# Kernel tuning notes

Measured on AMD Instinct MI355X. Metric: run time of the kernel, lower is better.

The kernel has to match this reference:

```python
import jax, jax.numpy as jnp
import numpy as np
import math

EPS_LN = 1e-5
SCALE = 16.0  # cosine_sim_scale


def layer_norm(x, g):
    mean = jnp.mean(x, axis=-1, keepdims=True)
    var = jnp.var(x, axis=-1, keepdims=True)  # biased, matches unbiased=False
    return (x - mean) * jax.lax.rsqrt(var + EPS_LN) * g


def l2norm(t):
    n = jnp.linalg.norm(t, axis=-1, keepdims=True)
    return t / jnp.maximum(n, 1e-12)


def setup_inputs() -> dict:
    key = jax.random.key(0)
    ks = jax.random.split(key, 4)
    b, n, dim, h, dh = 4, 2048, 1024, 8, 64
    inner = h * dh
    x = jax.random.normal(ks[0], (b, n, dim), dtype=jnp.float32)
    Wq = jax.random.normal(ks[1], (dim, inner), dtype=jnp.float32) * (dim ** -0.5)
    Wkv = jax.random.normal(ks[2], (dim, 2 * dh), dtype=jnp.float32) * (dim ** -0.5)
    Wout = jax.random.normal(ks[3], (inner, dim), dtype=jnp.float32) * (inner ** -0.5)
    norm_g = jnp.ones((dim,), dtype=jnp.float32)
    out_norm_g = jnp.ones((dim,), dtype=jnp.float32)
    return {"x": x, "norm_g": norm_g, "Wq": Wq, "Wkv": Wkv, "Wout": Wout,
            "out_norm_g": out_norm_g}


def reference(x, norm_g, Wq, Wkv, Wout, out_norm_g):
    b, n, dim = x.shape
    h = 8
    dh = Wkv.shape[-1] // 2
    xn = layer_norm(x, norm_g)
    q = xn @ Wq                      # [b, n, h*dh]
    kv = xn @ Wkv                    # [b, n, 2*dh]
    k, v = kv[..., :dh], kv[..., dh:]
    q = q.reshape(b, n, h, dh).transpose(0, 2, 1, 3)  # [b, h, n, dh]
    q = q * SCALE                    # cancelled by l2norm, kept for fidelity
    q = l2norm(q)
    k = l2norm(k)
    rs = math.sqrt(SCALE)
    q = q * rs
    k = k * rs
    sim = jnp.einsum('bhid,bjd->bhij', q, k)          # [b, h, n, n]
    attn = jax.nn.softmax(sim.astype(jnp.float32), axis=-1).astype(sim.dtype)
    out = jnp.einsum('bhij,bjd->bhid', attn, v)       # [b, h, n, dh]
    out = out.transpose(0, 2, 1, 3).reshape(b, n, h * dh)
    out = out @ Wout
    return layer_norm(out, out_norm_g)
```

## Files before the change

### kernel.cpp

```cpp
#include <hip/hip_runtime.h>
#include <hip/hip_bf16.h>

typedef __attribute__((ext_vector_type(8))) short short8;
typedef __attribute__((ext_vector_type(4))) float floatx4;

__device__ __forceinline__ float bf2f(ushort u) {
    return __uint_as_float(((unsigned int)u) << 16);
}
__device__ __forceinline__ ushort f2bf(float f) {
    unsigned int u = __float_as_uint(f);
    unsigned int r = (u + 0x7FFFu + ((u >> 16) & 1u)) >> 16;
    return (ushort)r;
}
__device__ __forceinline__ unsigned int pk2(float a, float b) {
    union { __hip_bfloat162 h; unsigned int u; } cv;
    cv.h = __float22bfloat162_rn(make_float2(a, b));
    return cv.u;
}
__device__ __forceinline__ float scrub(float v, float lim) {
    return fminf(fmaxf(v, -lim), lim);
}

__device__ __forceinline__ bool detect_bf16(const ushort* __restrict__ probe) {
    const int lane = threadIdx.x & 63;
    ushort u = probe[(lane & 31) * 2];
    int e = (u >> 7) & 0xFF;
    bool pl = (e >= 117) && (e <= 131) && (lane < 32);
    return __popcll(__ballot(pl)) >= 16;
}

__global__ __launch_bounds__(256) void ln1_kernel(const void* __restrict__ xin,
                                                  const void* __restrict__ gin,
                                                  ushort* __restrict__ out,
                                                  const ushort* __restrict__ probe) {
    const bool ib = detect_bf16(probe);
    const int row = blockIdx.x;
    const int tid = threadIdx.x;

    float v0, v1, v2, v3, g0, g1, g2, g3;
    if (ib) {
        uint2 u = *(const uint2*)((const ushort*)xin + (size_t)row * 1024 + tid * 4);
        v0 = bf2f((ushort)(u.x & 0xFFFF)); v1 = bf2f((ushort)(u.x >> 16));
        v2 = bf2f((ushort)(u.y & 0xFFFF)); v3 = bf2f((ushort)(u.y >> 16));
        uint2 gu = *(const uint2*)((const ushort*)gin + tid * 4);
        g0 = bf2f((ushort)(gu.x & 0xFFFF)); g1 = bf2f((ushort)(gu.x >> 16));
        g2 = bf2f((ushort)(gu.y & 0xFFFF)); g3 = bf2f((ushort)(gu.y >> 16));
    } else {
        float4 xv = *(const float4*)((const float*)xin + (size_t)row * 1024 + tid * 4);
        v0 = xv.x; v1 = xv.y; v2 = xv.z; v3 = xv.w;
        float4 gv = *(const float4*)((const float*)gin + tid * 4);
        g0 = gv.x; g1 = gv.y; g2 = gv.z; g3 = gv.w;
    }
    v0 = scrub(v0, 1e8f); v1 = scrub(v1, 1e8f); v2 = scrub(v2, 1e8f); v3 = scrub(v3, 1e8f);
    g0 = scrub(g0, 1e8f); g1 = scrub(g1, 1e8f); g2 = scrub(g2, 1e8f); g3 = scrub(g3, 1e8f);

    float s  = v0 + v1 + v2 + v3;
    float sq = v0 * v0 + v1 * v1 + v2 * v2 + v3 * v3;
    #pragma unroll
    for (int off = 1; off < 64; off <<= 1) {
        s  += __shfl_xor(s, off);
        sq += __shfl_xor(sq, off);
    }
    __shared__ float red[8];
    const int w = tid >> 6, lane = tid & 63;
    if (lane == 0) { red[w] = s; red[w + 4] = sq; }
    __syncthreads();
    float S  = red[0] + red[1] + red[2] + red[3];
    float SQ = red[4] + red[5] + red[6] + red[7];

    float mean = S * (1.0f / 1024.0f);
    float var  = SQ * (1.0f / 1024.0f) - mean * mean;
    float rstd = rsqrtf(fmaxf(var, 0.0f) + 1e-5f);

    uint2 ov;
    ov.x = pk2((v0 - mean) * rstd * g0, (v1 - mean) * rstd * g1);
    ov.y = pk2((v2 - mean) * rstd * g2, (v3 - mean) * rstd * g3);
    *(uint2*)(out + (size_t)row * 1024 + tid * 4) = ov;
}

__global__ __launch_bounds__(256) void ln2_kernel(const ushort* __restrict__ y,
                                                  const void* __restrict__ gin,
                                                  void* __restrict__ out,
                                                  const ushort* __restrict__ probe) {
    const bool ob = detect_bf16(probe);
    const int row = blockIdx.x;
    const int tid = threadIdx.x;

    uint2 u = *(const uint2*)(y + (size_t)row * 1024 + tid * 4);
    float v0 = scrub(bf2f((ushort)(u.x & 0xFFFF)), 1e8f);
    float v1 = scrub(bf2f((ushort)(u.x >> 16)),    1e8f);
    float v2 = scrub(bf2f((ushort)(u.y & 0xFFFF)), 1e8f);
    float v3 = scrub(bf2f((ushort)(u.y >> 16)),    1e8f);

    float g0, g1, g2, g3;
    if (ob) {
        uint2 gu = *(const uint2*)((const ushort*)gin + tid * 4);
        g0 = bf2f((ushort)(gu.x & 0xFFFF)); g1 = bf2f((ushort)(gu.x >> 16));
        g2 = bf2f((ushort)(gu.y & 0xFFFF)); g3 = bf2f((ushort)(gu.y >> 16));
    } else {
        float4 gv = *(const float4*)((const float*)gin + tid * 4);
        g0 = gv.x; g1 = gv.y; g2 = gv.z; g3 = gv.w;
    }
    g0 = scrub(g0, 1e8f); g1 = scrub(g1, 1e8f); g2 = scrub(g2, 1e8f); g3 = scrub(g3, 1e8f);

    float s  = v0 + v1 + v2 + v3;
    float sq = v0 * v0 + v1 * v1 + v2 * v2 + v3 * v3;
    #pragma unroll
    for (int off = 1; off < 64; off <<= 1) {
        s  += __shfl_xor(s, off);
        sq += __shfl_xor(sq, off);
    }
    __shared__ float red[8];
    const int w = tid >> 6, lane = tid & 63;
    if (lane == 0) { red[w] = s; red[w + 4] = sq; }
    __syncthreads();
    float S  = red[0] + red[1] + red[2] + red[3];
    float SQ = red[4] + red[5] + red[6] + red[7];

    float mean = S * (1.0f / 1024.0f);
    float var  = SQ * (1.0f / 1024.0f) - mean * mean;
    float rstd = rsqrtf(fmaxf(var, 0.0f) + 1e-5f);

    float o0 = (v0 - mean) * rstd * g0;
    float o1 = (v1 - mean) * rstd * g1;
    float o2 = (v2 - mean) * rstd * g2;
    float o3 = (v3 - mean) * rstd * g3;
    if (ob) {
        uint2 ov;
        ov.x = pk2(o0, o1);
        ov.y = pk2(o2, o3);
        *(uint2*)((ushort*)out + (size_t)row * 1024 + tid * 4) = ov;
    } else {
        *(float4*)((float*)out + (size_t)row * 1024 + tid * 4) = make_float4(o0, o1, o2, o3);
    }
}

__global__ __launch_bounds__(256) void transpose_kernel(const void* __restrict__ in,
                                                        ushort* __restrict__ out,
                                                        int in_rs, long long in_bs,
                                                        int out_rs, long long out_bs,
                                                        int force_bf16,
                                                        const ushort* __restrict__ probe) {
    const bool ib = force_bf16 ? true : detect_bf16(probe);
    __shared__ ushort tile[32][33];
    const int tx = threadIdx.x & 31, ty = threadIdx.x >> 5;

    #pragma unroll
    for (int rr = 0; rr < 32; rr += 8) {
        size_t idx = (size_t)blockIdx.z * in_bs + (size_t)(blockIdx.y * 32 + ty + rr) * in_rs
                   + blockIdx.x * 32 + tx;
        float v = ib ? bf2f(((const ushort*)in)[idx]) : ((const float*)in)[idx];
        tile[ty + rr][tx] = f2bf(scrub(v, 1e8f));
    }
    __syncthreads();
    ushort* op = out + (size_t)blockIdx.z * out_bs;
    #pragma unroll
    for (int rr = 0; rr < 32; rr += 8) {
        int r = blockIdx.x * 32 + ty + rr;
        int c = blockIdx.y * 32 + tx;
        op[(size_t)r * out_rs + c] = tile[tx][ty + rr];
    }
}

__global__ __launch_bounds__(256) void gemm_qkv(const ushort* __restrict__ A,
                                                const ushort* __restrict__ Bt,
                                                ushort* __restrict__ qb,
                                                ushort* __restrict__ kb,
                                                ushort* __restrict__ vt) {
    __shared__ ushort a_t[64][40];
    __shared__ ushort b_t[64][40];

    const int bx = blockIdx.x;
    const int n0 = bx * 64, m0 = blockIdx.y * 64;
    const int tid = threadIdx.x;
    const int w = tid >> 6, lane = tid & 63;
    const int fm = lane & 15, quad = lane >> 4;
    const int lrow = tid >> 2, lk = (tid & 3) * 8;
    const int K = 1024;

    const ushort* ag = A + (size_t)(m0 + lrow) * K + lk;
    const ushort* bg = Bt + (size_t)(n0 + lrow) * K + lk;

    floatx4 acc[4];
    floatx4 zero4 = {0.0f, 0.0f, 0.0f, 0.0f};
    #pragma unroll
    for (int nt = 0; nt < 4; nt++) acc[nt] = zero4;

    for (int k0 = 0; k0 < K; k0 += 32) {
        uint4 av = *(const uint4*)(ag + k0);
        uint4 bv = *(const uint4*)(bg + k0);
        __syncthreads();
        *(uint2*)&a_t[lrow][lk]     = make_uint2(av.x, av.y);
        *(uint2*)&a_t[lrow][lk + 4] = make_uint2(av.z, av.w);
        *(uint2*)&b_t[lrow][lk]     = make_uint2(bv.x, bv.y);
        *(uint2*)&b_t[lrow][lk + 4] = make_uint2(bv.z, bv.w);
        __syncthreads();

        union { uint2 u2[2]; short8 s8; } af;
        af.u2[0] = *(const uint2*)&a_t[w * 16 + fm][quad * 8];
        af.u2[1] = *(const uint2*)&a_t[w * 16 + fm][quad * 8 + 4];
        #pragma unroll
        for (int nt = 0; nt < 4; nt++) {
            union { uint2 u2[2]; short8 s8; } bf;
            bf.u2[0] = *(const uint2*)&b_t[nt * 16 + fm][quad * 8];
            bf.u2[1] = *(const uint2*)&b_t[nt * 16 + fm][quad * 8 + 4];
            acc[nt] = __builtin_amdgcn_mfma_f32_16x16x32_bf16(af.s8, bf.s8, acc[nt], 0, 0, 0);
        }
    }

    if (bx < 9) {
        float sc[4];
        #pragma unroll
        for (int r = 0; r < 4; r++) {
            float ss = acc[0][r] * acc[0][r] + acc[1][r] * acc[1][r]
                     + acc[2][r] * acc[2][r] + acc[3][r] * acc[3][r];
            ss += __shfl_xor(ss, 1);
            ss += __shfl_xor(ss, 2);
            ss += __shfl_xor(ss, 4);
            ss += __shfl_xor(ss, 8);
            sc[r] = 4.0f / fmaxf(sqrtf(ss), 1e-12f);
        }
        ushort* op;
        int rs;
        if (bx < 8) { op = qb + n0; rs = 512; }
        else        { op = kb;      rs = 64;  }
        #pragma unroll
        for (int nt = 0; nt < 4; nt++)
            #pragma unroll
            for (int r = 0; r < 4; r++)
                op[(size_t)(m0 + w * 16 + quad * 4 + r) * rs + nt * 16 + fm] =
                    f2bf(acc[nt][r] * sc[r]);
    } else {
        const int b = m0 >> 11;
        const int jb = (m0 & 2047) + w * 16 + quad * 4;
        ushort* vb = vt + (size_t)b * 64 * 2048 + jb;
        #pragma unroll
        for (int nt = 0; nt < 4; nt++) {
            uint2 pv;
            pv.x = pk2(acc[nt][0], acc[nt][1]);
            pv.y = pk2(acc[nt][2], acc[nt][3]);
            *(uint2*)(vb + (size_t)(nt * 16 + fm) * 2048) = pv;
        }
    }
}

__global__ __launch_bounds__(256) void gemm_bt(const ushort* __restrict__ A,
                                               const ushort* __restrict__ Bt,
                                               ushort* __restrict__ C,
                                               int M, int N, int K) {
    __shared__ ushort a_t[64][40];
    __shared__ ushort b_t[64][40];

    const int n0 = blockIdx.x * 64, m0 = blockIdx.y * 64;
    const int tid = threadIdx.x;
    const int w = tid >> 6, lane = tid & 63;
    const int fm = lane & 15, quad = lane >> 4;
    const int lrow = tid >> 2, lk = (tid & 3) * 8;

    const ushort* ag = A + (size_t)(m0 + lrow) * K + lk;
    const ushort* bg = Bt + (size_t)(n0 + lrow) * K + lk;

    floatx4 acc[4];
    floatx4 zero4 = {0.0f, 0.0f, 0.0f, 0.0f};
    #pragma unroll
    for (int nt = 0; nt < 4; nt++) acc[nt] = zero4;

    for (int k0 = 0; k0 < K; k0 += 32) {
        uint4 av = *(const uint4*)(ag + k0);
        uint4 bv = *(const uint4*)(bg + k0);
        __syncthreads();
        *(uint2*)&a_t[lrow][lk]     = make_uint2(av.x, av.y);
        *(uint2*)&a_t[lrow][lk + 4] = make_uint2(av.z, av.w);
        *(uint2*)&b_t[lrow][lk]     = make_uint2(bv.x, bv.y);
        *(uint2*)&b_t[lrow][lk + 4] = make_uint2(bv.z, bv.w);
        __syncthreads();

        union { uint2 u2[2]; short8 s8; } af;
        af.u2[0] = *(const uint2*)&a_t[w * 16 + fm][quad * 8];
        af.u2[1] = *(const uint2*)&a_t[w * 16 + fm][quad * 8 + 4];
        #pragma unroll
        for (int nt = 0; nt < 4; nt++) {
            union { uint2 u2[2]; short8 s8; } bf;
            bf.u2[0] = *(const uint2*)&b_t[nt * 16 + fm][quad * 8];
            bf.u2[1] = *(const uint2*)&b_t[nt * 16 + fm][quad * 8 + 4];
            acc[nt] = __builtin_amdgcn_mfma_f32_16x16x32_bf16(af.s8, bf.s8, acc[nt], 0, 0, 0);
        }
    }

    #pragma unroll
    for (int nt = 0; nt < 4; nt++)
        #pragma unroll
        for (int r = 0; r < 4; r++)
            C[(size_t)(m0 + w * 16 + quad * 4 + r) * N + n0 + nt * 16 + fm] = f2bf(acc[nt][r]);
}

__global__ __launch_bounds__(512, 4) void attn_kernel(const ushort* __restrict__ q,
                                                      const ushort* __restrict__ kb,
                                                      const ushort* __restrict__ vt,
                                                      ushort* __restrict__ out) {
    __shared__ ushort k_t[64][72];
    __shared__ ushort v_t[64][72];
    __shared__ ushort p_tile[8][16][72];

    const int i0 = blockIdx.x * 128;
    const int h = blockIdx.y, b = blockIdx.z;
    const int tid = threadIdx.x, w = tid >> 6, lane = tid & 63;
    const int fm = lane & 15, quad = lane >> 4;

    union U8 { uint4 u4; short8 s8; };

    const ushort* qbase = q + ((size_t)(b * 2048 + i0 + w * 16 + fm) * 512) + h * 64 + quad * 8;
    U8 qf0, qf1;
    qf0.u4 = *(const uint4*)qbase;
    qf1.u4 = *(const uint4*)(qbase + 32);

    floatx4 zero4 = {0.0f, 0.0f, 0.0f, 0.0f};
    floatx4 acc_o[4];
    #pragma unroll
    for (int od = 0; od < 4; od++) acc_o[od] = zero4;
    float lsum = 0.0f;

    const ushort* kbb = kb + (size_t)b * 2048 * 64;
    const ushort* vtb = vt + (size_t)b * 64 * 2048;

    const int srow = tid >> 3;
    const int sk = (tid & 7) * 8;

    for (int j0 = 0; j0 < 2048; j0 += 64) {
        uint4 ka = *(const uint4*)(kbb + (size_t)(j0 + srow) * 64 + sk);
        uint4 va = *(const uint4*)(vtb + (size_t)srow * 2048 + j0 + sk);
        __syncthreads();
        *(uint4*)&k_t[srow][sk] = ka;
        *(uint4*)&v_t[srow][sk] = va;
        __syncthreads();

        #pragma unroll
        for (int nt = 0; nt < 4; nt++) {
            U8 kb0, kb1;
            kb0.u4 = *(const uint4*)&k_t[nt * 16 + fm][quad * 8];
            kb1.u4 = *(const uint4*)&k_t[nt * 16 + fm][quad * 8 + 32];
            floatx4 st = zero4;
            st = __builtin_amdgcn_mfma_f32_16x16x32_bf16(kb0.s8, qf0.s8, st, 0, 0, 0);
            st = __builtin_amdgcn_mfma_f32_16x16x32_bf16(kb1.s8, qf1.s8, st, 0, 0, 0);
            float p0 = __expf(fminf(st[0], 16.0f) - 16.0f);
            float p1 = __expf(fminf(st[1], 16.0f) - 16.0f);
            float p2 = __expf(fminf(st[2], 16.0f) - 16.0f);
            float p3 = __expf(fminf(st[3], 16.0f) - 16.0f);
            lsum += (p0 + p1) + (p2 + p3);
            uint2 pkv;
            pkv.x = pk2(p0, p1);
            pkv.y = pk2(p2, p3);
            *(uint2*)&p_tile[w][fm][nt * 16 + quad * 4] = pkv;
        }

        U8 pb0, pb1;
        pb0.u4 = *(const uint4*)&p_tile[w][fm][quad * 8];
        pb1.u4 = *(const uint4*)&p_tile[w][fm][32 + quad * 8];

        #pragma unroll
        for (int od = 0; od < 4; od++) {
            U8 vb0, vb1;
            vb0.u4 = *(const uint4*)&v_t[od * 16 + fm][quad * 8];
            vb1.u4 = *(const uint4*)&v_t[od * 16 + fm][quad * 8 + 32];
            acc_o[od] = __builtin_amdgcn_mfma_f32_16x16x32_bf16(vb0.s8, pb0.s8, acc_o[od], 0, 0, 0);
            acc_o[od] = __builtin_amdgcn_mfma_f32_16x16x32_bf16(vb1.s8, pb1.s8, acc_o[od], 0, 0, 0);
        }
    }

    lsum += __shfl_xor(lsum, 16);
    lsum += __shfl_xor(lsum, 32);
    float li = 1.0f / fmaxf(lsum, 1e-30f);

    ushort* ob = out + (size_t)(b * 2048 + i0 + w * 16 + fm) * 512 + h * 64;
    #pragma unroll
    for (int od = 0; od < 4; od++) {
        uint2 ov;
        ov.x = pk2(acc_o[od][0] * li, acc_o[od][1] * li);
        ov.y = pk2(acc_o[od][2] * li, acc_o[od][3] * li);
        *(uint2*)(ob + od * 16 + quad * 4) = ov;
    }
}

extern "C" void kernel_launch(void* const* d_in, const int* in_sizes, int n_in,
                              void* d_out, int out_size, void* d_ws, size_t ws_size,
                              hipStream_t stream) {
    const void* x          = d_in[0];
    const void* norm_g     = d_in[1];
    const void* Wq         = d_in[2];
    const void* Wkv        = d_in[3];
    const void* Wout       = d_in[4];
    const void* out_norm_g = d_in[5];
    const ushort* probe = (const ushort*)d_in[0];
    ushort* ws = (ushort*)d_ws;

    const size_t M1 = 1024 * 1024 / 2;
    ushort* xn    = (ushort*)d_out;
    ushort* ao    = (ushort*)d_out;
    ushort* woT   = (ushort*)((char*)d_out + (8u << 20));
    ushort* qb    = ws;
    ushort* kb    = ws + 8 * M1;
    ushort* vt    = ws + 9 * M1;
    ushort* wcatT = ws + 11 * M1;
    ushort* y     = ws;

    transpose_kernel<<<dim3(16, 32, 1), 256, 0, stream>>>(Wq, wcatT, 512, 0, 1024, 0, 0, probe);
    transpose_kernel<<<dim3(4, 32, 1), 256, 0, stream>>>(Wkv, wcatT + (size_t)512 * 1024, 128, 0, 1024, 0, 0, probe);

    ln1_kernel<<<8192, 256, 0, stream>>>(x, norm_g, xn, probe);

    gemm_qkv<<<dim3(10, 128), 256, 0, stream>>>(xn, wcatT, qb, kb, vt);

    transpose_kernel<<<dim3(32, 16, 1), 256, 0, stream>>>(Wout, woT, 1024, 0, 512, 0, 0, probe);

    attn_kernel<<<dim3(16, 8, 4), 512, 0, stream>>>(qb, kb, vt, ao);

    gemm_bt<<<dim3(16, 128), 256, 0, stream>>>(ao, woT, y, 8192, 1024, 512);

    ln2_kernel<<<8192, 256, 0, stream>>>(y, out_norm_g, d_out, probe);
}
```

Before: 230.0 us.

## Fuse weight transposes into LN and attention kernels, enlarge output GEMM tiles

Weight transposes for Wq/Wkv are folded into the first layernorm launch and the Wout transpose into extra blocks of the attention launch, cutting the launch count. The output projection GEMM moves to 128x128 tiles fed by direct global-to-LDS loads. The attention loop now processes 128 keys per stage, and the clamp before exp is dropped, which relies on scores staying at or below 16 after l2norm. These changes reduce launch overhead and synchronisation per unit of work but raise LDS use per block and remove the overflow guard.

```diff
diff --git a/kernel.cpp b/kernel.cpp
--- a/kernel.cpp
+++ b/kernel.cpp
@@ -19,6 +19,10 @@
 }
 __device__ __forceinline__ float scrub(float v, float lim) {
     return fminf(fmaxf(v, -lim), lim);
+}
+__device__ __forceinline__ void glds16(const ushort* g, ushort* l) {
+    __builtin_amdgcn_global_load_lds((const __attribute__((address_space(1))) void*)g,
+                                     (__attribute__((address_space(3))) void*)l, 16, 0, 0);
 }
 
 __device__ __forceinline__ bool detect_bf16(const ushort* __restrict__ probe) {
@@ -29,14 +33,50 @@
     return __popcll(__ballot(pl)) >= 16;
 }
 
-__global__ __launch_bounds__(256) void ln1_kernel(const void* __restrict__ xin,
-                                                  const void* __restrict__ gin,
-                                                  ushort* __restrict__ out,
-                                                  const ushort* __restrict__ probe) {
+__device__ __forceinline__ void do_transpose(const void* __restrict__ in,
+                                             ushort* __restrict__ out,
+                                             int bx, int by, int in_rs, int out_rs,
+                                             bool ib, ushort* tile , int nthr) {
+    const int tx = threadIdx.x & 31, ty = threadIdx.x >> 5;
+    const int step = nthr >> 5;
+    for (int rr = 0; rr < 32; rr += step) {
+        size_t idx = (size_t)(by * 32 + ty + rr) * in_rs + bx * 32 + tx;
+        float v = ib ? bf2f(((const ushort*)in)[idx]) : ((const float*)in)[idx];
+        tile[(ty + rr) * 33 + tx] = f2bf(scrub(v, 1e8f));
+    }
+    __syncthreads();
+    for (int rr = 0; rr < 32; rr += step) {
+        int r = bx * 32 + ty + rr;
+        int c = by * 32 + tx;
+        out[(size_t)r * out_rs + c] = tile[tx * 33 + (ty + rr)];
+    }
+}
+
+__global__ __launch_bounds__(256) void prep_kernel(const void* __restrict__ xin,
+                                                   const void* __restrict__ gin,
+                                                   const void* __restrict__ Wq,
+                                                   const void* __restrict__ Wkv,
+                                                   ushort* __restrict__ xn,
+                                                   ushort* __restrict__ wcatT,
+                                                   const ushort* __restrict__ probe) {
     const bool ib = detect_bf16(probe);
-    const int row = blockIdx.x;
+    const int id = blockIdx.x;
+    __shared__ ushort tile[32 * 33];
+    __shared__ float red[8];
+
+    if (id >= 8192) {
+        if (id < 8704) {
+            int t = id - 8192;
+            do_transpose(Wq, wcatT, t & 15, t >> 4, 512, 1024, ib, tile, 256);
+        } else {
+            int t = id - 8704;
+            do_transpose(Wkv, wcatT + (size_t)512 * 1024, t & 3, t >> 2, 128, 1024, ib, tile, 256);
+        }
+        return;
+    }
+
+    const int row = id;
     const int tid = threadIdx.x;
-
     float v0, v1, v2, v3, g0, g1, g2, g3;
     if (ib) {
         uint2 u = *(const uint2*)((const ushort*)xin + (size_t)row * 1024 + tid * 4);
@@ -61,7 +101,6 @@
         s  += __shfl_xor(s, off);
         sq += __shfl_xor(sq, off);
     }
-    __shared__ float red[8];
     const int w = tid >> 6, lane = tid & 63;
     if (lane == 0) { red[w] = s; red[w + 4] = sq; }
     __syncthreads();
@@ -75,7 +114,7 @@
     uint2 ov;
     ov.x = pk2((v0 - mean) * rstd * g0, (v1 - mean) * rstd * g1);
     ov.y = pk2((v2 - mean) * rstd * g2, (v3 - mean) * rstd * g3);
-    *(uint2*)(out + (size_t)row * 1024 + tid * 4) = ov;
+    *(uint2*)(xn + (size_t)row * 1024 + tid * 4) = ov;
 }
 
 __global__ __launch_bounds__(256) void ln2_kernel(const ushort* __restrict__ y,
@@ -135,33 +174,6 @@
     }
 }
 
-__global__ __launch_bounds__(256) void transpose_kernel(const void* __restrict__ in,
-                                                        ushort* __restrict__ out,
-                                                        int in_rs, long long in_bs,
-                                                        int out_rs, long long out_bs,
-                                                        int force_bf16,
-                                                        const ushort* __restrict__ probe) {
-    const bool ib = force_bf16 ? true : detect_bf16(probe);
-    __shared__ ushort tile[32][33];
-    const int tx = threadIdx.x & 31, ty = threadIdx.x >> 5;
-
-    #pragma unroll
-    for (int rr = 0; rr < 32; rr += 8) {
-        size_t idx = (size_t)blockIdx.z * in_bs + (size_t)(blockIdx.y * 32 + ty + rr) * in_rs
-                   + blockIdx.x * 32 + tx;
-        float v = ib ? bf2f(((const ushort*)in)[idx]) : ((const float*)in)[idx];
-        tile[ty + rr][tx] = f2bf(scrub(v, 1e8f));
-    }
-    __syncthreads();
-    ushort* op = out + (size_t)blockIdx.z * out_bs;
-    #pragma unroll
-    for (int rr = 0; rr < 32; rr += 8) {
-        int r = blockIdx.x * 32 + ty + rr;
-        int c = blockIdx.y * 32 + tx;
-        op[(size_t)r * out_rs + c] = tile[tx][ty + rr];
-    }
-}
-
 __global__ __launch_bounds__(256) void gemm_qkv(const ushort* __restrict__ A,
                                                 const ushort* __restrict__ Bt,
                                                 ushort* __restrict__ qb,
@@ -244,63 +256,85 @@
     }
 }
 
-__global__ __launch_bounds__(256) void gemm_bt(const ushort* __restrict__ A,
-                                               const ushort* __restrict__ Bt,
-                                               ushort* __restrict__ C,
-                                               int M, int N, int K) {
-    __shared__ ushort a_t[64][40];
-    __shared__ ushort b_t[64][40];
-
-    const int n0 = blockIdx.x * 64, m0 = blockIdx.y * 64;
+__global__ __launch_bounds__(256) void gemm_bt128(const ushort* __restrict__ A,
+                                                  const ushort* __restrict__ Bt,
+                                                  ushort* __restrict__ C,
+                                                  int M, int N, int K) {
+    __shared__ ushort a_t[128][32];
+    __shared__ ushort b_t[128][32];
+
+    const int n0 = blockIdx.x * 128, m0 = blockIdx.y * 128;
     const int tid = threadIdx.x;
     const int w = tid >> 6, lane = tid & 63;
     const int fm = lane & 15, quad = lane >> 4;
-    const int lrow = tid >> 2, lk = (tid & 3) * 8;
-
-    const ushort* ag = A + (size_t)(m0 + lrow) * K + lk;
-    const ushort* bg = Bt + (size_t)(n0 + lrow) * K + lk;
-
-    floatx4 acc[4];
+
+    const int c0 = tid, c1 = tid + 256;
+    const ushort* ag0 = A + (size_t)(m0 + (c0 >> 2)) * K + (c0 & 3) * 8;
+    const ushort* ag1 = A + (size_t)(m0 + (c1 >> 2)) * K + (c1 & 3) * 8;
+    const ushort* bg0 = Bt + (size_t)(n0 + (c0 >> 2)) * K + (c0 & 3) * 8;
+    const ushort* bg1 = Bt + (size_t)(n0 + (c1 >> 2)) * K + (c1 & 3) * 8;
+    ushort* la0 = &a_t[0][0] + c0 * 8;
+    ushort* la1 = &a_t[0][0] + c1 * 8;
+    ushort* lb0 = &b_t[0][0] + c0 * 8;
+    ushort* lb1 = &b_t[0][0] + c1 * 8;
+
+    floatx4 acc[2][8];
     floatx4 zero4 = {0.0f, 0.0f, 0.0f, 0.0f};
     #pragma unroll
-    for (int nt = 0; nt < 4; nt++) acc[nt] = zero4;
+    for (int mt = 0; mt < 2; mt++)
+        #pragma unroll
+        for (int nt = 0; nt < 8; nt++) acc[mt][nt] = zero4;
+
+    union U8 { uint4 u4; short8 s8; };
 
     for (int k0 = 0; k0 < K; k0 += 32) {
-        uint4 av = *(const uint4*)(ag + k0);
-        uint4 bv = *(const uint4*)(bg + k0);
-        __syncthreads();
-        *(uint2*)&a_t[lrow][lk]     = make_uint2(av.x, av.y);
-        *(uint2*)&a_t[lrow][lk + 4] = make_uint2(av.z, av.w);
-        *(uint2*)&b_t[lrow][lk]     = make_uint2(bv.x, bv.y);
-        *(uint2*)&b_t[lrow][lk + 4] = make_uint2(bv.z, bv.w);
-        __syncthreads();
-
-        union { uint2 u2[2]; short8 s8; } af;
-        af.u2[0] = *(const uint2*)&a_t[w * 16 + fm][quad * 8];
-        af.u2[1] = *(const uint2*)&a_t[w * 16 + fm][quad * 8 + 4];
-        #pragma unroll
-        for (int nt = 0; nt < 4; nt++) {
-            union { uint2 u2[2]; short8 s8; } bf;
-            bf.u2[0] = *(const uint2*)&b_t[nt * 16 + fm][quad * 8];
-            bf.u2[1] = *(const uint2*)&b_t[nt * 16 + fm][quad * 8 + 4];
-            acc[nt] = __builtin_amdgcn_mfma_f32_16x16x32_bf16(af.s8, bf.s8, acc[nt], 0, 0, 0);
-        }
-    }
-
-    #pragma unroll
-    for (int nt = 0; nt < 4; nt++)
-        #pragma unroll
-        for (int r = 0; r < 4; r++)
-            C[(size_t)(m0 + w * 16 + quad * 4 + r) * N + n0 + nt * 16 + fm] = f2bf(acc[nt][r]);
+        __syncthreads();
+        glds16(ag0 + k0, la0);
+        glds16(ag1 + k0, la1);
+        glds16(bg0 + k0, lb0);
+        glds16(bg1 + k0, lb1);
+        __syncthreads();
+
+        U8 af[2];
+        #pragma unroll
+        for (int mt = 0; mt < 2; mt++)
+            af[mt].u4 = *(const uint4*)&a_t[w * 32 + mt * 16 + fm][quad * 8];
+        #pragma unroll
+        for (int nt = 0; nt < 8; nt++) {
+            U8 bf;
+            bf.u4 = *(const uint4*)&b_t[nt * 16 + fm][quad * 8];
+            acc[0][nt] = __builtin_amdgcn_mfma_f32_16x16x32_bf16(af[0].s8, bf.s8, acc[0][nt], 0, 0, 0);
+            acc[1][nt] = __builtin_amdgcn_mfma_f32_16x16x32_bf16(af[1].s8, bf.s8, acc[1][nt], 0, 0, 0);
+        }
+    }
+
+    #pragma unroll
+    for (int mt = 0; mt < 2; mt++)
+        #pragma unroll
+        for (int nt = 0; nt < 8; nt++)
+            #pragma unroll
+            for (int r = 0; r < 4; r++)
+                C[(size_t)(m0 + w * 32 + mt * 16 + quad * 4 + r) * N + n0 + nt * 16 + fm] =
+                    f2bf(acc[mt][nt][r]);
 }
 
 __global__ __launch_bounds__(512, 4) void attn_kernel(const ushort* __restrict__ q,
                                                       const ushort* __restrict__ kb,
                                                       const ushort* __restrict__ vt,
-                                                      ushort* __restrict__ out) {
-    __shared__ ushort k_t[64][72];
-    __shared__ ushort v_t[64][72];
+                                                      ushort* __restrict__ out,
+                                                      const void* __restrict__ Wout,
+                                                      ushort* __restrict__ woT,
+                                                      const ushort* __restrict__ probe) {
+    __shared__ ushort k_t[128][72];
+    __shared__ ushort v_t[64][136];
     __shared__ ushort p_tile[8][16][72];
+
+    if (blockIdx.x >= 16) {
+        const bool ib = detect_bf16(probe);
+        int id = (blockIdx.x - 16) + 16 * (blockIdx.y + 8 * blockIdx.z);
+        do_transpose(Wout, woT, id & 31, id >> 5, 1024, 512, ib, &k_t[0][0], 512);
+        return;
+    }
 
     const int i0 = blockIdx.x * 128;
     const int h = blockIdx.y, b = blockIdx.z;
@@ -323,47 +357,55 @@
     const ushort* kbb = kb + (size_t)b * 2048 * 64;
     const ushort* vtb = vt + (size_t)b * 64 * 2048;
 
-    const int srow = tid >> 3;
-    const int sk = (tid & 7) * 8;
-
-    for (int j0 = 0; j0 < 2048; j0 += 64) {
-        uint4 ka = *(const uint4*)(kbb + (size_t)(j0 + srow) * 64 + sk);
-        uint4 va = *(const uint4*)(vtb + (size_t)srow * 2048 + j0 + sk);
-        __syncthreads();
-        *(uint4*)&k_t[srow][sk] = ka;
-        *(uint4*)&v_t[srow][sk] = va;
-        __syncthreads();
-
-        #pragma unroll
-        for (int nt = 0; nt < 4; nt++) {
-            U8 kb0, kb1;
-            kb0.u4 = *(const uint4*)&k_t[nt * 16 + fm][quad * 8];
-            kb1.u4 = *(const uint4*)&k_t[nt * 16 + fm][quad * 8 + 32];
-            floatx4 st = zero4;
-            st = __builtin_amdgcn_mfma_f32_16x16x32_bf16(kb0.s8, qf0.s8, st, 0, 0, 0);
-            st = __builtin_amdgcn_mfma_f32_16x16x32_bf16(kb1.s8, qf1.s8, st, 0, 0, 0);
-            float p0 = __expf(fminf(st[0], 16.0f) - 16.0f);
-            float p1 = __expf(fminf(st[1], 16.0f) - 16.0f);
-            float p2 = __expf(fminf(st[2], 16.0f) - 16.0f);
-            float p3 = __expf(fminf(st[3], 16.0f) - 16.0f);
-            lsum += (p0 + p1) + (p2 + p3);
-            uint2 pkv;
-            pkv.x = pk2(p0, p1);
-            pkv.y = pk2(p2, p3);
-            *(uint2*)&p_tile[w][fm][nt * 16 + quad * 4] = pkv;
-        }
-
-        U8 pb0, pb1;
-        pb0.u4 = *(const uint4*)&p_tile[w][fm][quad * 8];
-        pb1.u4 = *(const uint4*)&p_tile[w][fm][32 + quad * 8];
-
-        #pragma unroll
-        for (int od = 0; od < 4; od++) {
-            U8 vb0, vb1;
-            vb0.u4 = *(const uint4*)&v_t[od * 16 + fm][quad * 8];
-            vb1.u4 = *(const uint4*)&v_t[od * 16 + fm][quad * 8 + 32];
-            acc_o[od] = __builtin_amdgcn_mfma_f32_16x16x32_bf16(vb0.s8, pb0.s8, acc_o[od], 0, 0, 0);
-            acc_o[od] = __builtin_amdgcn_mfma_f32_16x16x32_bf16(vb1.s8, pb1.s8, acc_o[od], 0, 0, 0);
+    const int srow = tid >> 3, sk = (tid & 7) * 8;
+    const int vrow = tid >> 4, vk = (tid & 15) * 8;
+
+    for (int j0 = 0; j0 < 2048; j0 += 128) {
+        uint4 ka0 = *(const uint4*)(kbb + (size_t)(j0 + srow) * 64 + sk);
+        uint4 ka1 = *(const uint4*)(kbb + (size_t)(j0 + srow + 64) * 64 + sk);
+        uint4 va0 = *(const uint4*)(vtb + (size_t)vrow * 2048 + j0 + vk);
+        uint4 va1 = *(const uint4*)(vtb + (size_t)(vrow + 32) * 2048 + j0 + vk);
+        __syncthreads();
+        *(uint4*)&k_t[srow][sk]      = ka0;
+        *(uint4*)&k_t[srow + 64][sk] = ka1;
+        *(uint4*)&v_t[vrow][vk]      = va0;
+        *(uint4*)&v_t[vrow + 32][vk] = va1;
+        __syncthreads();
+
+        #pragma unroll
+        for (int half = 0; half < 2; half++) {
+            const int jj = half * 64;
+            #pragma unroll
+            for (int nt = 0; nt < 4; nt++) {
+                U8 kf0, kf1;
+                kf0.u4 = *(const uint4*)&k_t[jj + nt * 16 + fm][quad * 8];
+                kf1.u4 = *(const uint4*)&k_t[jj + nt * 16 + fm][quad * 8 + 32];
+                floatx4 st = zero4;
+                st = __builtin_amdgcn_mfma_f32_16x16x32_bf16(kf0.s8, qf0.s8, st, 0, 0, 0);
+                st = __builtin_amdgcn_mfma_f32_16x16x32_bf16(kf1.s8, qf1.s8, st, 0, 0, 0);
+                float p0 = __expf(st[0] - 16.0f);
+                float p1 = __expf(st[1] - 16.0f);
+                float p2 = __expf(st[2] - 16.0f);
+                float p3 = __expf(st[3] - 16.0f);
+                lsum += (p0 + p1) + (p2 + p3);
+                uint2 pkv;
+                pkv.x = pk2(p0, p1);
+                pkv.y = pk2(p2, p3);
+                *(uint2*)&p_tile[w][fm][nt * 16 + quad * 4] = pkv;
+            }
+
+            U8 pb0, pb1;
+            pb0.u4 = *(const uint4*)&p_tile[w][fm][quad * 8];
+            pb1.u4 = *(const uint4*)&p_tile[w][fm][32 + quad * 8];
+
+            #pragma unroll
+            for (int od = 0; od < 4; od++) {
+                U8 vf0, vf1;
+                vf0.u4 = *(const uint4*)&v_t[od * 16 + fm][jj + quad * 8];
+                vf1.u4 = *(const uint4*)&v_t[od * 16 + fm][jj + quad * 8 + 32];
+                acc_o[od] = __builtin_amdgcn_mfma_f32_16x16x32_bf16(vf0.s8, pb0.s8, acc_o[od], 0, 0, 0);
+                acc_o[od] = __builtin_amdgcn_mfma_f32_16x16x32_bf16(vf1.s8, pb1.s8, acc_o[od], 0, 0, 0);
+            }
         }
     }
 
@@ -403,18 +445,13 @@
     ushort* wcatT = ws + 11 * M1;
     ushort* y     = ws;
 
-    transpose_kernel<<<dim3(16, 32, 1), 256, 0, stream>>>(Wq, wcatT, 512, 0, 1024, 0, 0, probe);
-    transpose_kernel<<<dim3(4, 32, 1), 256, 0, stream>>>(Wkv, wcatT + (size_t)512 * 1024, 128, 0, 1024, 0, 0, probe);
-
-    ln1_kernel<<<8192, 256, 0, stream>>>(x, norm_g, xn, probe);
+    prep_kernel<<<8832, 256, 0, stream>>>(x, norm_g, Wq, Wkv, xn, wcatT, probe);
 
     gemm_qkv<<<dim3(10, 128), 256, 0, stream>>>(xn, wcatT, qb, kb, vt);
 
-    transpose_kernel<<<dim3(32, 16, 1), 256, 0, stream>>>(Wout, woT, 1024, 0, 512, 0, 0, probe);
-
-    attn_kernel<<<dim3(16, 8, 4), 512, 0, stream>>>(qb, kb, vt, ao);
-
-    gemm_bt<<<dim3(16, 128), 256, 0, stream>>>(ao, woT, y, 8192, 1024, 512);
+    attn_kernel<<<dim3(32, 8, 4), 512, 0, stream>>>(qb, kb, vt, ao, Wout, woT, probe);
+
+    gemm_bt128<<<dim3(8, 64), 256, 0, stream>>>(ao, woT, y, 8192, 1024, 512);
 
     ln2_kernel<<<8192, 256, 0, stream>>>(y, out_norm_g, d_out, probe);
 }
```

Result: slower. 259.1 us (+12.7%).
